# Performance work log

Hardware: AMD Instinct MI355X
Metric: run time of the kernel (lower is better)

## Reference

```python
import jax, jax.numpy as jnp
import numpy as np
from jax.ops import segment_sum

N_PFAS, N_GW, N_SW = 50000, 200000, 20000
D_IN, D_OUT, D_EDGE = 32, 32, 3
E_PG, E_GP, E_PS, E_SP = 2000000, 2000000, 1000000, 1000000


def _params(key):
    ks = jax.random.split(key, 24)
    g = lambda k, s: jax.random.normal(k, s, dtype=jnp.float32) * 0.05
    p = {}
    # SAGEConvWithEdgeAttr for pg (pfas->gw) and gp (gw->pfas)
    for i, rel in enumerate(['pg', 'gp']):
        o = i * 5
        p[f'Wl_{rel}'] = g(ks[o + 0], (D_IN, D_OUT))
        p[f'bl_{rel}'] = g(ks[o + 1], (D_OUT,))
        p[f'Wr_{rel}'] = g(ks[o + 2], (D_IN, D_OUT))
        p[f'We_{rel}'] = g(ks[o + 3], (D_EDGE, D_OUT))
        p[f'be_{rel}'] = g(ks[o + 4], (D_OUT,))
    # plain SAGEConv for ps (pfas->sw) and sp (sw->pfas)
    for i, rel in enumerate(['ps', 'sp']):
        o = 10 + i * 3
        p[f'Wl_{rel}'] = g(ks[o + 0], (D_IN, D_OUT))
        p[f'bl_{rel}'] = g(ks[o + 1], (D_OUT,))
        p[f'Wr_{rel}'] = g(ks[o + 2], (D_IN, D_OUT))
    p['W_out'] = g(ks[16], (D_OUT, 1))
    p['b_out'] = g(ks[17], (1,))
    p['a_prelu'] = jnp.float32(0.25) * jnp.ones((1,), jnp.float32)
    return p


def setup_inputs() -> dict:
    key = jax.random.key(0)
    ks = jax.random.split(key, 16)
    inp = {
        'x_pfas': jax.random.normal(ks[0], (N_PFAS, D_IN), jnp.float32),
        'x_gw': jax.random.normal(ks[1], (N_GW, D_IN), jnp.float32),
        'x_sw': jax.random.normal(ks[2], (N_SW, D_IN), jnp.float32),
        'src_pg': jax.random.randint(ks[3], (E_PG,), 0, N_PFAS),
        'dst_pg': jax.random.randint(ks[4], (E_PG,), 0, N_GW),
        'ea_pg': jax.random.uniform(ks[5], (E_PG, D_EDGE), jnp.float32),
        'src_gp': jax.random.randint(ks[6], (E_GP,), 0, N_GW),
        'dst_gp': jax.random.randint(ks[7], (E_GP,), 0, N_PFAS),
        'ea_gp': jax.random.uniform(ks[8], (E_GP, D_EDGE), jnp.float32),
        'src_ps': jax.random.randint(ks[9], (E_PS,), 0, N_PFAS),
        'dst_ps': jax.random.randint(ks[10], (E_PS,), 0, N_SW),
        'src_sp': jax.random.randint(ks[11], (E_SP,), 0, N_SW),
        'dst_sp': jax.random.randint(ks[12], (E_SP,), 0, N_PFAS),
    }
    inp.update(_params(ks[13]))
    return inp


def _sage(x_src, x_dst, src, dst, Wl, bl, Wr, n_dst):
    # PyG SAGEConv: lin_l(mean_aggr(x_j)) + lin_r(x_dst); lin_r has no bias
    msg = x_src[src]                                   # [E, D_IN]
    s = segment_sum(msg, dst, num_segments=n_dst)      # [n_dst, D_IN]
    cnt = segment_sum(jnp.ones((src.shape[0],), x_src.dtype), dst, num_segments=n_dst)
    mean = s / jnp.maximum(cnt, 1.0)[:, None]
    return mean @ Wl + bl + x_dst @ Wr


def _edge_scatter_set(dst, ea_t, n_dst):
    # matches torch zeros.scatter_(0, col, edge_attr_transformed): overwrite at dst
    return jnp.zeros((n_dst, ea_t.shape[1]), ea_t.dtype).at[dst].set(ea_t)


def reference(x_pfas, x_gw, x_sw,
              src_pg, dst_pg, ea_pg,
              src_gp, dst_gp, ea_gp,
              src_ps, dst_ps, src_sp, dst_sp,
              Wl_pg, bl_pg, Wr_pg, We_pg, be_pg,
              Wl_gp, bl_gp, Wr_gp, We_gp, be_gp,
              Wl_ps, bl_ps, Wr_ps,
              Wl_sp, bl_sp, Wr_sp,
              W_out, b_out, a_prelu):
    # pfas -> gw (edge attrs)
    out_gw = _sage(x_pfas, x_gw, src_pg, dst_pg, Wl_pg, bl_pg, Wr_pg, N_GW)
    out_gw = out_gw + _edge_scatter_set(dst_pg, ea_pg @ We_pg + be_pg, N_GW)
    # gw -> pfas (edge attrs)
    out_pf1 = _sage(x_gw, x_pfas, src_gp, dst_gp, Wl_gp, bl_gp, Wr_gp, N_PFAS)
    out_pf1 = out_pf1 + _edge_scatter_set(dst_gp, ea_gp @ We_gp + be_gp, N_PFAS)
    # sw -> pfas (plain SAGE)
    out_pf2 = _sage(x_sw, x_pfas, src_sp, dst_sp, Wl_sp, bl_sp, Wr_sp, N_PFAS)
    # pfas -> sw (plain SAGE)
    out_sw = _sage(x_pfas, x_sw, src_ps, dst_ps, Wl_ps, bl_ps, Wr_ps, N_SW)
    # HeteroConv aggr='sum' over relations with same dst type, then relu
    h_pfas = jax.nn.relu(out_pf1 + out_pf2)
    h_gw = jax.nn.relu(out_gw)
    h_sw = jax.nn.relu(out_sw)
    # final linear + PReLU on gw_wells
    y = h_gw @ W_out + b_out                           # [N_GW, 1]
    y = jnp.where(y >= 0, y, a_prelu * y)
    return h_pfas, y, h_sw
```

## Files before the change

### kernel.cpp

```cpp
#include <hip/hip_runtime.h>
#include <hip/hip_fp16.h>

typedef unsigned int u32;
typedef unsigned long long u64;

#define NPFAS 50000
#define NGW   200000
#define NSW   20000
#define D     32
#define EPG   2000000
#define EGP   2000000
#define EPS   1000000
#define ESP   1000000

#define NB_PG 782
#define NB_GP 782
#define NB_SP 391
#define NB_PS 313
#define CAP_PG 2880
#define CAP_GP 2880
#define CAP_SP 2880
#define CAP_PS 3584
#define SORT_MAX 3584

#define ZGCUR    0
#define MAXE_PG  2304
#define MAXE_GP  202304
#define S_PG     252304
#define S_GP     6652304
#define S_SP     8252304
#define S_PS     9852304
#define CNT_PG   10492304
#define CNT_GP   10692304
#define CNT_SP   10742304
#define CNT_PS   10792304
#define REG_PG   10812304
#define REG_GP   15316624
#define REG_SP   19820944
#define REG_PS   20947024
#define XH_PFAS  22068816
#define XH_GW    22868816

#define PART_BLOCKS 512
#define CONV_BLOCKS 256

__device__ __forceinline__ void part4_narrow(
    const int* __restrict__ src, const int* __restrict__ dst,
    int e0, int e1, int nb, int cp, int cf, int pshift, int bbits, int roundSz,
    u32* __restrict__ region, int cap, int* __restrict__ gcur,
    u32* binData, u32* binCnt)
{
    u32 dlm = (1u << bbits) - 1u;
    for (int b = threadIdx.x; b < nb; b += 256) binCnt[b] = 0;
    __syncthreads();
    for (int base = e0; base < e1; base += roundSz) {
        int rend = base + roundSz; if (rend > e1) rend = e1;
        for (int e = base + (int)threadIdx.x; e < rend; e += 256) {
            int d = dst[e];
            int bk = d >> bbits;
            u32 w0 = (u32)src[e] | (((u32)d & dlm) << pshift);
            u32 pos = atomicAdd(&binCnt[bk], 1u);
            if ((int)pos < cp) {
                binData[bk * cp + (int)pos] = w0;
            } else {
                int g = atomicAdd(&gcur[bk], 1);
                if (g < cap) region[(size_t)bk * cap + g] = w0;
            }
        }
        __syncthreads();
        bool last = (base + roundSz >= e1);
        for (int b = threadIdx.x; b < nb; b += 256) {
            int c = (int)binCnt[b];
            if (c > cp) c = cp;
            if (c >= cf || (last && c > 0)) {
                int g = atomicAdd(&gcur[b], c);
                int lim = cap - g; if (lim < 0) lim = 0; if (c > lim) c = lim;
                u32* dp = region + ((size_t)b * cap + g);
                for (int i = 0; i < c; i++) dp[i] = binData[b * cp + i];
                binCnt[b] = 0;
            }
        }
        __syncthreads();
    }
}

__device__ __forceinline__ void part4_wide(
    const int* __restrict__ src, const int* __restrict__ dst,
    int e0, int e1, int nb, int cp, int cf, int bbits, int roundSz,
    u64* __restrict__ region, int cap, int* __restrict__ gcur,
    u64* binData, u32* binCnt)
{
    u32 dlm = (1u << bbits) - 1u;
    for (int b = threadIdx.x; b < nb; b += 256) binCnt[b] = 0;
    __syncthreads();
    for (int base = e0; base < e1; base += roundSz) {
        int rend = base + roundSz; if (rend > e1) rend = e1;
        for (int e = base + (int)threadIdx.x; e < rend; e += 256) {
            int d = dst[e];
            int bk = d >> bbits;
            u64 w0 = ((u64)(u32)e << 32) | (u32)src[e] | (((u32)d & dlm) << 21);
            u32 pos = atomicAdd(&binCnt[bk], 1u);
            if ((int)pos < cp) {
                binData[bk * cp + (int)pos] = w0;
            } else {
                int g = atomicAdd(&gcur[bk], 1);
                if (g < cap) region[(size_t)bk * cap + g] = w0;
            }
        }
        __syncthreads();
        bool last = (base + roundSz >= e1);
        for (int b = threadIdx.x; b < nb; b += 256) {
            int c = (int)binCnt[b];
            if (c > cp) c = cp;
            if (c >= cf || (last && c > 0)) {
                int g = atomicAdd(&gcur[b], c);
                int lim = cap - g; if (lim < 0) lim = 0; if (c > lim) c = lim;
                u64* dp = region + ((size_t)b * cap + g);
                for (int i = 0; i < c; i++) dp[i] = binData[b * cp + i];
                binCnt[b] = 0;
            }
        }
        __syncthreads();
    }
}

__global__ __launch_bounds__(256) void partition_conv(
    const int* __restrict__ src_pg, const int* __restrict__ dst_pg,
    const int* __restrict__ src_gp, const int* __restrict__ dst_gp,
    const int* __restrict__ src_sp, const int* __restrict__ dst_sp,
    const int* __restrict__ src_ps, const int* __restrict__ dst_ps,
    const float* __restrict__ x_pfas, const float* __restrict__ x_gw,
    int* __restrict__ wsi)
{
    __shared__ __align__(16) u64 binData64[6256];
    __shared__ u32 binCnt[782];
    u32* ws = (u32*)wsi;
    int b = blockIdx.x;
    if (b >= PART_BLOCKS) {
        __half2* hp = (__half2*)(wsi + XH_PFAS);
        __half2* hg = (__half2*)(wsi + XH_GW);
        const float2* fp = (const float2*)x_pfas;
        const float2* fg = (const float2*)x_gw;
        int idx = (b - PART_BLOCKS) * 256 + (int)threadIdx.x;
        const int NTP = NPFAS * D / 2;
        const int NTT = NTP + NGW * D / 2;
        for (int i = idx; i < NTT; i += CONV_BLOCKS * 256) {
            if (i < NTP) {
                float2 v = fp[i];
                hp[i] = __floats2half2_rn(v.x, v.y);
            } else {
                float2 v = fg[i - NTP];
                hg[i - NTP] = __floats2half2_rn(v.x, v.y);
            }
        }
        return;
    }
    if (b < 160) {
        int e0 = b * (EPG / 160);
        part4_wide(src_pg, dst_pg, e0, e0 + EPG / 160, NB_PG, 8, 6, 8, 2048,
                   (u64*)(ws + REG_PG), CAP_PG, wsi + ZGCUR + 0, binData64, binCnt);
    } else if (b < 320) {
        int bb = b - 160;
        int e0 = bb * (EGP / 160);
        part4_wide(src_gp, dst_gp, e0, e0 + EGP / 160, NB_GP, 8, 6, 6, 2048,
                   (u64*)(ws + REG_GP), CAP_GP, wsi + ZGCUR + 782, binData64, binCnt);
    } else if (b < 416) {
        int bb = b - 320;
        int e0 = (int)(((long long)bb * ESP) / 96);
        int e1 = (int)(((long long)(bb + 1) * ESP) / 96);
        part4_narrow(src_sp, dst_sp, e0, e1, NB_SP, 32, 24, 15, 7, 2048,
                     ws + REG_SP, CAP_SP, wsi + ZGCUR + 1564, (u32*)binData64, binCnt);
    } else {
        int bb = b - 416;
        int e0 = (int)(((long long)bb * EPS) / 96);
        int e1 = (int)(((long long)(bb + 1) * EPS) / 96);
        part4_narrow(src_ps, dst_ps, e0, e1, NB_PS, 32, 24, 16, 6, 2048,
                     ws + REG_PS, CAP_PS, wsi + ZGCUR + 1955, (u32*)binData64, binCnt);
    }
}

__global__ __launch_bounds__(256) void sort_agg(
    const float* __restrict__ x_sw,
    int* __restrict__ wsi)
{
    __shared__ u32 sortedS[SORT_MAX];
    __shared__ int histS[256];
    __shared__ int startS[256];
    __shared__ int cursorS[256];
    __shared__ int mxS[256];
    __shared__ int wsum[4];

    float* wsf = (float*)wsi;
    u32* wsu = (u32*)wsi;
    int tid = threadIdx.x;
    int bid = blockIdx.x;

    const __half2* xh2 = nullptr; const float2* xf2 = nullptr;
    const u64* reg64 = nullptr; const u32* reg32 = nullptr;
    int gi, cap, pshift, nbDst, dbase, ndst;
    u32 smask; bool wide; float* sOut; float* cntOut; int* mxOut = nullptr;

    if (bid < NB_PG) {
        xh2 = (const __half2*)(wsi + XH_PFAS);
        reg64 = (const u64*)(wsu + REG_PG) + (size_t)bid * CAP_PG; gi = ZGCUR + bid;
        cap = CAP_PG; pshift = 21; smask = 0x1FFFFFu; wide = true;
        nbDst = 256; dbase = bid << 8; ndst = NGW;
        sOut = wsf + S_PG; cntOut = wsf + CNT_PG; mxOut = wsi + MAXE_PG;
    } else if (bid < NB_PG + NB_GP) {
        int b = bid - NB_PG;
        xh2 = (const __half2*)(wsi + XH_GW);
        reg64 = (const u64*)(wsu + REG_GP) + (size_t)b * CAP_GP; gi = ZGCUR + 782 + b;
        cap = CAP_GP; pshift = 21; smask = 0x1FFFFFu; wide = true;
        nbDst = 64; dbase = b << 6; ndst = NPFAS;
        sOut = wsf + S_GP; cntOut = wsf + CNT_GP; mxOut = wsi + MAXE_GP;
    } else if (bid < NB_PG + NB_GP + NB_SP) {
        int b = bid - NB_PG - NB_GP;
        xf2 = (const float2*)x_sw;
        reg32 = wsu + REG_SP + (size_t)b * CAP_SP; gi = ZGCUR + 1564 + b;
        cap = CAP_SP; pshift = 15; smask = 0x7FFFu; wide = false;
        nbDst = 128; dbase = b << 7; ndst = NPFAS;
        sOut = wsf + S_SP; cntOut = wsf + CNT_SP;
    } else {
        int b = bid - NB_PG - NB_GP - NB_SP;
        xh2 = (const __half2*)(wsi + XH_PFAS);
        reg32 = wsu + REG_PS + (size_t)b * CAP_PS; gi = ZGCUR + 1955 + b;
        cap = CAP_PS; pshift = 16; smask = 0xFFFFu; wide = false;
        nbDst = 64; dbase = b << 6; ndst = NSW;
        sOut = wsf + S_PS; cntOut = wsf + CNT_PS;
    }

    int nEnt = wsi[gi]; if (nEnt > cap) nEnt = cap;

    histS[tid] = 0;
    mxS[tid] = -1;
    __syncthreads();

    if (wide) {
        for (int i = tid; i < nEnt; i += 256) {
            u64 w = reg64[i];
            int dl = (int)(((u32)w >> 21) & 255u);
            atomicAdd(&histS[dl], 1);
            atomicMax(&mxS[dl], (int)(u32)(w >> 32));
        }
    } else {
        for (int i = tid; i < nEnt; i += 256) {
            u32 w = reg32[i];
            int dl = (int)((w >> pshift) & 255u);
            atomicAdd(&histS[dl], 1);
        }
    }
    __syncthreads();

    {
        int v = histS[tid];
        int lane = tid & 63, w = tid >> 6;
        int incl = v;
#pragma unroll
        for (int off = 1; off < 64; off <<= 1) {
            int t = __shfl_up(incl, off);
            if (lane >= off) incl += t;
        }
        if (lane == 63) wsum[w] = incl;
        startS[tid] = incl - v;
    }
    __syncthreads();
    {
        int w = tid >> 6;
        int off = 0;
        for (int k = 0; k < w; k++) off += wsum[k];
        int st = startS[tid] + off;
        startS[tid] = st;
        cursorS[tid] = st;
    }
    __syncthreads();

    if (wide) {
        for (int i = tid; i < nEnt; i += 256) {
            u64 w = reg64[i];
            int dl = (int)(((u32)w >> 21) & 255u);
            int pos = atomicAdd(&cursorS[dl], 1);
            if (pos < SORT_MAX) sortedS[pos] = (u32)w & smask;
        }
    } else {
        for (int i = tid; i < nEnt; i += 256) {
            u32 w = reg32[i];
            int dl = (int)((w >> pshift) & 255u);
            int pos = atomicAdd(&cursorS[dl], 1);
            if (pos < SORT_MAX) sortedS[pos] = w & smask;
        }
    }
    __syncthreads();

    int wv = tid >> 6, lane = tid & 63;
    int half32 = lane >> 5;
    int l32 = lane & 31;
    int rs = l32 >> 4;
    int fp = l32 & 15;
    for (int q0 = wv * 2; q0 < nbDst; q0 += 8) {
        int q = q0 + half32;
        int dn = dbase + q;
        bool valid = (q < nbDst) && (dn < ndst);
        int deg = valid ? histS[q] : 0;
        int p0 = valid ? startS[q] : 0;
        float ax = 0.f, ay = 0.f;
        int i = 0;
        if (xh2) {
            for (; i + 7 < deg; i += 8) {
                int s0 = (int)sortedS[p0 + i + rs];
                int s1 = (int)sortedS[p0 + i + 2 + rs];
                int s2 = (int)sortedS[p0 + i + 4 + rs];
                int s3 = (int)sortedS[p0 + i + 6 + rs];
                float2 f0 = __half22float2(xh2[s0 * 16 + fp]);
                float2 f1 = __half22float2(xh2[s1 * 16 + fp]);
                float2 f2 = __half22float2(xh2[s2 * 16 + fp]);
                float2 f3 = __half22float2(xh2[s3 * 16 + fp]);
                ax += (f0.x + f1.x) + (f2.x + f3.x);
                ay += (f0.y + f1.y) + (f2.y + f3.y);
            }
            for (; i < deg; i += 2) {
                if (i + rs < deg) {
                    float2 f0 = __half22float2(xh2[(int)sortedS[p0 + i + rs] * 16 + fp]);
                    ax += f0.x; ay += f0.y;
                }
            }
        } else {
            for (; i + 7 < deg; i += 8) {
                int s0 = (int)sortedS[p0 + i + rs];
                int s1 = (int)sortedS[p0 + i + 2 + rs];
                int s2 = (int)sortedS[p0 + i + 4 + rs];
                int s3 = (int)sortedS[p0 + i + 6 + rs];
                float2 f0 = xf2[s0 * 16 + fp];
                float2 f1 = xf2[s1 * 16 + fp];
                float2 f2 = xf2[s2 * 16 + fp];
                float2 f3 = xf2[s3 * 16 + fp];
                ax += (f0.x + f1.x) + (f2.x + f3.x);
                ay += (f0.y + f1.y) + (f2.y + f3.y);
            }
            for (; i < deg; i += 2) {
                if (i + rs < deg) {
                    float2 f0 = xf2[(int)sortedS[p0 + i + rs] * 16 + fp];
                    ax += f0.x; ay += f0.y;
                }
            }
        }
        ax += __shfl_xor(ax, 16); ay += __shfl_xor(ay, 16);
        if (valid && rs == 0) {
            float2* so2 = (float2*)(sOut + (size_t)dn * D);
            so2[fp] = make_float2(ax, ay);
        }
        if (valid && l32 == 0) {
            cntOut[dn] = (float)deg;
            if (wide) mxOut[dn] = mxS[q];
        }
    }
}

#define GW_B   782
#define PFAS_B 196
#define SW_B   79

__global__ __launch_bounds__(256) void finalize_all(
    const float* __restrict__ s_pg, const float* __restrict__ cnt_pg,
    const int* __restrict__ maxe_pg, const float* __restrict__ x_gw,
    const float* __restrict__ ea_pg,
    const float* __restrict__ Wl_pg, const float* __restrict__ bl_pg,
    const float* __restrict__ Wr_pg, const float* __restrict__ We_pg,
    const float* __restrict__ be_pg,
    const float* __restrict__ W_out, const float* __restrict__ b_out,
    const float* __restrict__ a_prelu,
    const float* __restrict__ s_gp, const float* __restrict__ cnt_gp,
    const int* __restrict__ maxe_gp,
    const float* __restrict__ s_sp, const float* __restrict__ cnt_sp,
    const float* __restrict__ x_pfas, const float* __restrict__ ea_gp,
    const float* __restrict__ Wl_gp, const float* __restrict__ bl_gp,
    const float* __restrict__ Wr_gp, const float* __restrict__ We_gp,
    const float* __restrict__ be_gp,
    const float* __restrict__ Wl_sp, const float* __restrict__ bl_sp,
    const float* __restrict__ Wr_sp,
    const float* __restrict__ s_ps, const float* __restrict__ cnt_ps,
    const float* __restrict__ x_sw,
    const float* __restrict__ Wl_ps, const float* __restrict__ bl_ps,
    const float* __restrict__ Wr_ps,
    float* __restrict__ h_pfas, float* __restrict__ y_out, float* __restrict__ h_sw)
{
    __shared__ __align__(16) float sh[3328];
    int tid = threadIdx.x;
    int b = blockIdx.x;

    if (b < GW_B) {
        float* WlT = sh;
        float* WrT = sh + 1024;
        float* WeT = sh + 2048;
        float* blS = sh + 2144;
        float* beS = sh + 2176;
        float* WoS = sh + 2208;
        for (int i = tid; i < D * D; i += 256) {
            int k = i / D, j = i % D;
            WlT[j * D + k] = Wl_pg[i];
            WrT[j * D + k] = Wr_pg[i];
        }
        for (int i = tid; i < 3 * D; i += 256) {
            int k = i / D, j = i % D;
            WeT[j * 3 + k] = We_pg[i];
        }
        if (tid < D) {
            blS[tid] = bl_pg[tid];
            beS[tid] = be_pg[tid];
            WoS[tid] = W_out[tid];
        }
        __syncthreads();

        int n = b * 256 + tid;
        if (n >= NGW) return;

        float mean[D], xd[D];
        float inv = 1.0f / fmaxf(cnt_pg[n], 1.0f);
        const float4* sp = (const float4*)(s_pg + (size_t)n * D);
        const float4* xp = (const float4*)(x_gw + (size_t)n * D);
#pragma unroll
        for (int q = 0; q < D / 4; q++) {
            float4 sv = sp[q];
            mean[4*q+0] = sv.x * inv; mean[4*q+1] = sv.y * inv;
            mean[4*q+2] = sv.z * inv; mean[4*q+3] = sv.w * inv;
            float4 xv = xp[q];
            xd[4*q+0] = xv.x; xd[4*q+1] = xv.y; xd[4*q+2] = xv.z; xd[4*q+3] = xv.w;
        }
        int me = maxe_pg[n];
        bool he = (me >= 0);
        float e0 = 0.f, e1 = 0.f, e2 = 0.f;
        if (he) {
            e0 = ea_pg[(size_t)me * 3 + 0];
            e1 = ea_pg[(size_t)me * 3 + 1];
            e2 = ea_pg[(size_t)me * 3 + 2];
        }
        float yacc = 0.f;
        for (int j = 0; j < D; j++) {
            float o = blS[j] + (he ? beS[j] : 0.0f);
            const float4* wl4 = (const float4*)(WlT + j * D);
            const float4* wr4 = (const float4*)(WrT + j * D);
#pragma unroll
            for (int q = 0; q < D / 4; q++) {
                float4 wl = wl4[q], wr = wr4[q];
                o += mean[4*q+0]*wl.x + mean[4*q+1]*wl.y + mean[4*q+2]*wl.z + mean[4*q+3]*wl.w;
                o += xd[4*q+0]*wr.x + xd[4*q+1]*wr.y + xd[4*q+2]*wr.z + xd[4*q+3]*wr.w;
            }
            if (he) o += e0*WeT[j*3+0] + e1*WeT[j*3+1] + e2*WeT[j*3+2];
            float h = fmaxf(o, 0.0f);
            yacc += h * WoS[j];
        }
        float y = yacc + b_out[0];
        float ap = a_prelu[0];
        y_out[n] = (y >= 0.f) ? y : ap * y;

    } else if (b < GW_B + PFAS_B) {
        float* WlgT = sh;
        float* WlsT = sh + 1024;
        float* WrcT = sh + 2048;
        float* WeT  = sh + 3072;
        float* blc  = sh + 3168;
        float* beS  = sh + 3200;
        for (int i = tid; i < D * D; i += 256) {
            int k = i / D, j = i % D;
            WlgT[j * D + k] = Wl_gp[i];
            WlsT[j * D + k] = Wl_sp[i];
            WrcT[j * D + k] = Wr_gp[i] + Wr_sp[i];
        }
        for (int i = tid; i < 3 * D; i += 256) {
            int k = i / D, j = i % D;
            WeT[j * 3 + k] = We_gp[i];
        }
        if (tid < D) {
            blc[tid] = bl_gp[tid] + bl_sp[tid];
            beS[tid] = be_gp[tid];
        }
        __syncthreads();

        int n = (b - GW_B) * 256 + tid;
        if (n >= NPFAS) return;

        float mg[D], ms[D], xd[D];
        float invg = 1.0f / fmaxf(cnt_gp[n], 1.0f);
        float invs = 1.0f / fmaxf(cnt_sp[n], 1.0f);
        const float4* gp4 = (const float4*)(s_gp + (size_t)n * D);
        const float4* sp4 = (const float4*)(s_sp + (size_t)n * D);
        const float4* xp4 = (const float4*)(x_pfas + (size_t)n * D);
#pragma unroll
        for (int q = 0; q < D / 4; q++) {
            float4 a = gp4[q];
            mg[4*q+0] = a.x * invg; mg[4*q+1] = a.y * invg; mg[4*q+2] = a.z * invg; mg[4*q+3] = a.w * invg;
            float4 bb = sp4[q];
            ms[4*q+0] = bb.x * invs; ms[4*q+1] = bb.y * invs; ms[4*q+2] = bb.z * invs; ms[4*q+3] = bb.w * invs;
            float4 c = xp4[q];
            xd[4*q+0] = c.x; xd[4*q+1] = c.y; xd[4*q+2] = c.z; xd[4*q+3] = c.w;
        }
        int me = maxe_gp[n];
        bool he = (me >= 0);
        float e0 = 0.f, e1 = 0.f, e2 = 0.f;
        if (he) {
            e0 = ea_gp[(size_t)me * 3 + 0];
            e1 = ea_gp[(size_t)me * 3 + 1];
            e2 = ea_gp[(size_t)me * 3 + 2];
        }
        float* out = h_pfas + (size_t)n * D;
        for (int j = 0; j < D; j++) {
            float o = blc[j] + (he ? beS[j] : 0.0f);
            const float4* wg4 = (const float4*)(WlgT + j * D);
            const float4* ws4 = (const float4*)(WlsT + j * D);
            const float4* wc4 = (const float4*)(WrcT + j * D);
#pragma unroll
            for (int q = 0; q < D / 4; q++) {
                float4 wg = wg4[q], wsv = ws4[q], wc = wc4[q];
                o += mg[4*q+0]*wg.x + mg[4*q+1]*wg.y + mg[4*q+2]*wg.z + mg[4*q+3]*wg.w;
                o += ms[4*q+0]*wsv.x + ms[4*q+1]*wsv.y + ms[4*q+2]*wsv.z + ms[4*q+3]*wsv.w;
                o += xd[4*q+0]*wc.x + xd[4*q+1]*wc.y + xd[4*q+2]*wc.z + xd[4*q+3]*wc.w;
            }
            if (he) o += e0*WeT[j*3+0] + e1*WeT[j*3+1] + e2*WeT[j*3+2];
            out[j] = fmaxf(o, 0.0f);
        }

    } else {
        float* WlT = sh;
        float* WrT = sh + 1024;
        float* blS = sh + 2048;
        for (int i = tid; i < D * D; i += 256) {
            int k = i / D, j = i % D;
            WlT[j * D + k] = Wl_ps[i];
            WrT[j * D + k] = Wr_ps[i];
        }
        if (tid < D) blS[tid] = bl_ps[tid];
        __syncthreads();

        int n = (b - GW_B - PFAS_B) * 256 + tid;
        if (n >= NSW) return;

        float mean[D], xd[D];
        float inv = 1.0f / fmaxf(cnt_ps[n], 1.0f);
        const float4* sp = (const float4*)(s_ps + (size_t)n * D);
        const float4* xp = (const float4*)(x_sw + (size_t)n * D);
#pragma unroll
        for (int q = 0; q < D / 4; q++) {
            float4 sv = sp[q];
            mean[4*q+0] = sv.x * inv; mean[4*q+1] = sv.y * inv;
            mean[4*q+2] = sv.z * inv; mean[4*q+3] = sv.w * inv;
            float4 xv = xp[q];
            xd[4*q+0] = xv.x; xd[4*q+1] = xv.y; xd[4*q+2] = xv.z; xd[4*q+3] = xv.w;
        }
        float* out = h_sw + (size_t)n * D;
        for (int j = 0; j < D; j++) {
            float o = blS[j];
            const float4* wl4 = (const float4*)(WlT + j * D);
            const float4* wr4 = (const float4*)(WrT + j * D);
#pragma unroll
            for (int q = 0; q < D / 4; q++) {
                float4 wl = wl4[q], wr = wr4[q];
                o += mean[4*q+0]*wl.x + mean[4*q+1]*wl.y + mean[4*q+2]*wl.z + mean[4*q+3]*wl.w;
                o += xd[4*q+0]*wr.x + xd[4*q+1]*wr.y + xd[4*q+2]*wr.z + xd[4*q+3]*wr.w;
            }
            out[j] = fmaxf(o, 0.0f);
        }
    }
}

extern "C" void kernel_launch(void* const* d_in, const int* in_sizes, int n_in,
                              void* d_out, int out_size, void* d_ws, size_t ws_size,
                              hipStream_t stream) {
    (void)in_sizes; (void)n_in; (void)out_size; (void)ws_size;
    const float* x_pfas = (const float*)d_in[0];
    const float* x_gw   = (const float*)d_in[1];
    const float* x_sw   = (const float*)d_in[2];
    const int*   src_pg = (const int*)d_in[3];
    const int*   dst_pg = (const int*)d_in[4];
    const float* ea_pg  = (const float*)d_in[5];
    const int*   src_gp = (const int*)d_in[6];
    const int*   dst_gp = (const int*)d_in[7];
    const float* ea_gp  = (const float*)d_in[8];
    const int*   src_ps = (const int*)d_in[9];
    const int*   dst_ps = (const int*)d_in[10];
    const int*   src_sp = (const int*)d_in[11];
    const int*   dst_sp = (const int*)d_in[12];
    const float* Wl_pg = (const float*)d_in[13];
    const float* bl_pg = (const float*)d_in[14];
    const float* Wr_pg = (const float*)d_in[15];
    const float* We_pg = (const float*)d_in[16];
    const float* be_pg = (const float*)d_in[17];
    const float* Wl_gp = (const float*)d_in[18];
    const float* bl_gp = (const float*)d_in[19];
    const float* Wr_gp = (const float*)d_in[20];
    const float* We_gp = (const float*)d_in[21];
    const float* be_gp = (const float*)d_in[22];
    const float* Wl_ps = (const float*)d_in[23];
    const float* bl_ps = (const float*)d_in[24];
    const float* Wr_ps = (const float*)d_in[25];
    const float* Wl_sp = (const float*)d_in[26];
    const float* bl_sp = (const float*)d_in[27];
    const float* Wr_sp = (const float*)d_in[28];
    const float* W_out = (const float*)d_in[29];
    const float* b_out = (const float*)d_in[30];
    const float* a_pre = (const float*)d_in[31];

    int*   wsi = (int*)d_ws;
    float* wsf = (float*)d_ws;

    hipMemsetAsync(wsi + ZGCUR, 0, 2304 * sizeof(int), stream);

    partition_conv<<<PART_BLOCKS + CONV_BLOCKS, 256, 0, stream>>>(
        src_pg, dst_pg, src_gp, dst_gp,
        src_sp, dst_sp, src_ps, dst_ps,
        x_pfas, x_gw, wsi);

    sort_agg<<<NB_PG + NB_GP + NB_SP + NB_PS, 256, 0, stream>>>(x_sw, wsi);

    float* out    = (float*)d_out;
    float* h_pfas = out;
    float* y_out  = out + 1600000;
    float* h_sw   = out + 1800000;

    finalize_all<<<GW_B + PFAS_B + SW_B, 256, 0, stream>>>(
        wsf + S_PG, wsf + CNT_PG, wsi + MAXE_PG, x_gw, ea_pg,
        Wl_pg, bl_pg, Wr_pg, We_pg, be_pg, W_out, b_out, a_pre,
        wsf + S_GP, wsf + CNT_GP, wsi + MAXE_GP, wsf + S_SP, wsf + CNT_SP,
        x_pfas, ea_gp,
        Wl_gp, bl_gp, Wr_gp, We_gp, be_gp,
        Wl_sp, bl_sp, Wr_sp,
        wsf + S_PS, wsf + CNT_PS, x_sw, Wl_ps, bl_ps, Wr_ps,
        h_pfas, y_out, h_sw);
}
```

Baseline: 431.9 us.

## Split wide partition bins across two blocks to halve shared memory per block

Each wide partition block now covers only half of the destination bins (391 of 782), with two blocks reading the same edge chunk. Shared memory per block drops from about 53KB to about 26KB, which allows more resident blocks and raises the partition block count. The narrow-path staging per bin is also reduced (cp 32→16, flush threshold 24→8). The cost is that every edge index is read twice for the wide relations, and with smaller per-bin staging the global flushes become smaller and more frequent, with more global atomics.

```diff
diff --git a/kernel.cpp b/kernel.cpp
--- a/kernel.cpp
+++ b/kernel.cpp
@@ -41,7 +41,11 @@
 #define XH_PFAS  22068816
 #define XH_GW    22868816
 
-#define PART_BLOCKS 512
+#define PB_PG 256
+#define PB_GP 256
+#define PB_SP 128
+#define PB_PS 128
+#define PART_BLOCKS (PB_PG + PB_GP + PB_SP + PB_PS)
 #define CONV_BLOCKS 256
 
 __device__ __forceinline__ void part4_narrow(
@@ -86,7 +90,7 @@
 
 __device__ __forceinline__ void part4_wide(
     const int* __restrict__ src, const int* __restrict__ dst,
-    int e0, int e1, int nb, int cp, int cf, int bbits, int roundSz,
+    int e0, int e1, int bbase, int nb, int cp, int cf, int bbits, int roundSz,
     u64* __restrict__ region, int cap, int* __restrict__ gcur,
     u64* binData, u32* binCnt)
 {
@@ -97,14 +101,16 @@
         int rend = base + roundSz; if (rend > e1) rend = e1;
         for (int e = base + (int)threadIdx.x; e < rend; e += 256) {
             int d = dst[e];
-            int bk = d >> bbits;
-            u64 w0 = ((u64)(u32)e << 32) | (u32)src[e] | (((u32)d & dlm) << 21);
-            u32 pos = atomicAdd(&binCnt[bk], 1u);
-            if ((int)pos < cp) {
-                binData[bk * cp + (int)pos] = w0;
-            } else {
-                int g = atomicAdd(&gcur[bk], 1);
-                if (g < cap) region[(size_t)bk * cap + g] = w0;
+            int bk = (d >> bbits) - bbase;
+            if ((unsigned)bk < (unsigned)nb) {
+                u64 w0 = ((u64)(u32)e << 32) | (u32)src[e] | (((u32)d & dlm) << 21);
+                u32 pos = atomicAdd(&binCnt[bk], 1u);
+                if ((int)pos < cp) {
+                    binData[bk * cp + (int)pos] = w0;
+                } else {
+                    int g = atomicAdd(&gcur[bbase + bk], 1);
+                    if (g < cap) region[(size_t)(bbase + bk) * cap + g] = w0;
+                }
             }
         }
         __syncthreads();
@@ -113,9 +119,9 @@
             int c = (int)binCnt[b];
             if (c > cp) c = cp;
             if (c >= cf || (last && c > 0)) {
-                int g = atomicAdd(&gcur[b], c);
+                int g = atomicAdd(&gcur[bbase + b], c);
                 int lim = cap - g; if (lim < 0) lim = 0; if (c > lim) c = lim;
-                u64* dp = region + ((size_t)b * cap + g);
+                u64* dp = region + ((size_t)(bbase + b) * cap + g);
                 for (int i = 0; i < c; i++) dp[i] = binData[b * cp + i];
                 binCnt[b] = 0;
             }
@@ -132,8 +138,8 @@
     const float* __restrict__ x_pfas, const float* __restrict__ x_gw,
     int* __restrict__ wsi)
 {
-    __shared__ __align__(16) u64 binData64[6256];
-    __shared__ u32 binCnt[782];
+    __shared__ __align__(16) u64 binData64[3128];
+    __shared__ u32 binCnt[391];
     u32* ws = (u32*)wsi;
     int b = blockIdx.x;
     if (b >= PART_BLOCKS) {
@@ -155,26 +161,28 @@
         }
         return;
     }
-    if (b < 160) {
-        int e0 = b * (EPG / 160);
-        part4_wide(src_pg, dst_pg, e0, e0 + EPG / 160, NB_PG, 8, 6, 8, 2048,
+    if (b < PB_PG) {
+        int half = b & 1, chunk = b >> 1;
+        int e0 = chunk * (EPG / 128);
+        part4_wide(src_pg, dst_pg, e0, e0 + EPG / 128, half * 391, 391, 8, 6, 8, 2048,
                    (u64*)(ws + REG_PG), CAP_PG, wsi + ZGCUR + 0, binData64, binCnt);
-    } else if (b < 320) {
-        int bb = b - 160;
-        int e0 = bb * (EGP / 160);
-        part4_wide(src_gp, dst_gp, e0, e0 + EGP / 160, NB_GP, 8, 6, 6, 2048,
+    } else if (b < PB_PG + PB_GP) {
+        int bb = b - PB_PG;
+        int half = bb & 1, chunk = bb >> 1;
+        int e0 = chunk * (EGP / 128);
+        part4_wide(src_gp, dst_gp, e0, e0 + EGP / 128, half * 391, 391, 8, 6, 6, 2048,
                    (u64*)(ws + REG_GP), CAP_GP, wsi + ZGCUR + 782, binData64, binCnt);
-    } else if (b < 416) {
-        int bb = b - 320;
-        int e0 = (int)(((long long)bb * ESP) / 96);
-        int e1 = (int)(((long long)(bb + 1) * ESP) / 96);
-        part4_narrow(src_sp, dst_sp, e0, e1, NB_SP, 32, 24, 15, 7, 2048,
+    } else if (b < PB_PG + PB_GP + PB_SP) {
+        int bb = b - PB_PG - PB_GP;
+        int e0 = (int)(((long long)bb * ESP) / PB_SP);
+        int e1 = (int)(((long long)(bb + 1) * ESP) / PB_SP);
+        part4_narrow(src_sp, dst_sp, e0, e1, NB_SP, 16, 8, 15, 7, 2048,
                      ws + REG_SP, CAP_SP, wsi + ZGCUR + 1564, (u32*)binData64, binCnt);
     } else {
-        int bb = b - 416;
-        int e0 = (int)(((long long)bb * EPS) / 96);
-        int e1 = (int)(((long long)(bb + 1) * EPS) / 96);
-        part4_narrow(src_ps, dst_ps, e0, e1, NB_PS, 32, 24, 16, 6, 2048,
+        int bb = b - PB_PG - PB_GP - PB_SP;
+        int e0 = (int)(((long long)bb * EPS) / PB_PS);
+        int e1 = (int)(((long long)(bb + 1) * EPS) / PB_PS);
+        part4_narrow(src_ps, dst_ps, e0, e1, NB_PS, 16, 8, 16, 6, 2048,
                      ws + REG_PS, CAP_PS, wsi + ZGCUR + 1955, (u32*)binData64, binCnt);
     }
 }
```

Result: slower. 449.9 us (+4.2%).
